# Kernel optimization log

Hardware: AMD Instinct MI355X
Metric: run time of the kernel (lower is better)

## Reference

```python
import jax, jax.numpy as jnp
import numpy as np

EPS = 1e-6

def setup_inputs() -> dict:
    key = jax.random.key(0)
    ks = jax.random.split(key, 6)
    N, E, Din, H, D = 50000, 800000, 256, 4, 32
    x = jax.random.normal(ks[0], (N, Din), dtype=jnp.float32)
    adj_indices = jax.random.randint(ks[1], (E, 2), 0, N, dtype=jnp.int32)
    adj_weights = jax.random.uniform(ks[2], (E,), dtype=jnp.float32)
    W = jax.random.normal(ks[3], (Din, H * D), dtype=jnp.float32) * (1.0 / np.sqrt(Din))
    a_src = jax.random.normal(ks[4], (H, D), dtype=jnp.float32)
    a_dst = jax.random.normal(ks[5], (H, D), dtype=jnp.float32)
    return {"x": x, "adj_indices": adj_indices, "adj_weights": adj_weights,
            "W": W, "a_src": a_src, "a_dst": a_dst}

def reference(x, adj_indices, adj_weights, W, a_src, a_dst):
    N = x.shape[0]
    H, D = a_src.shape
    h = (x @ W).reshape(N, H, D)                       # [N,H,D]
    src = adj_indices[:, 0]
    dst = adj_indices[:, 1]
    hs = h[src]                                        # [E,H,D]
    hd = h[dst]                                        # [E,H,D]
    raw = jnp.einsum('ehd,hd->eh', hs, a_src) + jnp.einsum('ehd,hd->eh', hd, a_dst)
    gate = jnp.clip(adj_weights, EPS, None)[:, None]   # [E,1]
    scores = jnp.tanh(raw) + jnp.log(gate)             # [E,H]
    # per-destination segment softmax (numerically stable)
    seg_max = jax.ops.segment_max(scores, dst, num_segments=N)   # [N,H]
    ex = jnp.exp(scores - seg_max[dst])
    denom = jax.ops.segment_sum(ex, dst, num_segments=N)         # [N,H]
    alpha = ex / denom[dst]                            # softmax over edges per dst
    alpha = alpha * gate
    messages = alpha[:, :, None] * hs                  # [E,H,D]
    out = jax.ops.segment_sum(messages, dst, num_segments=N)     # [N,H,D]
    out = out.reshape(N, H * D)
    return jax.nn.gelu(out, approximate=False)
```

## Files before the change

kernel.cpp:

```cpp
#include <hip/hip_runtime.h>
#include <hip/hip_bf16.h>

#define N_NODES 50000
#define N_EDGES 800000
#define DIN 256
#define HD 128
#define NH 4
#define CAP 64

#define GROWS 64
#define LDK 264

#define GEMM_BLOCKS ((N_NODES + GROWS - 1) / GROWS)
#define SCAT_BLOCKS ((N_EDGES + 255) / 256)

typedef __bf16 bf16x8 __attribute__((ext_vector_type(8)));
typedef float  f32x4  __attribute__((ext_vector_type(4)));

static __device__ __forceinline__ unsigned short f2bu(float v) {
  union { __hip_bfloat16 b; unsigned short u; } c;
  c.b = __float2bfloat16(v);
  return c.u;
}

__global__ void init_kernel(const float* __restrict__ W,
                            unsigned short* __restrict__ Wt,
                            int* __restrict__ cursor) {
  int i = blockIdx.x * 256 + threadIdx.x;
  if (i < HD * DIN) {
    int c = i >> 8, k = i & 255;
    Wt[c * 256 + k] = f2bu(W[k * HD + c]);
  }
  if (i < N_NODES) cursor[i] = 0;
}

__global__ __launch_bounds__(256, 2) void fused_gemm_scatter(
    const float* __restrict__ x,
    const unsigned short* __restrict__ Wt,
    const float* __restrict__ a_src,
    const float* __restrict__ a_dst,
    unsigned short* __restrict__ hbf,
    float* __restrict__ ssrc,
    float* __restrict__ sdst,
    const int2* __restrict__ adj,
    const float* __restrict__ wts,
    int* __restrict__ cursor,
    int2* __restrict__ slots) {
  __shared__ unsigned short xs[GROWS * LDK];
  const int tid = threadIdx.x;

  if (blockIdx.x >= GEMM_BLOCKS) {
    int e = (blockIdx.x - GEMM_BLOCKS) * 256 + tid;
    if (e >= N_EDGES) return;
    int2 sd = adj[e];
    if ((unsigned)sd.x >= (unsigned)N_NODES || (unsigned)sd.y >= (unsigned)N_NODES) return;
    float g = fmaxf(wts[e], 1e-6f);
    int pos = atomicAdd(&cursor[sd.y], 1);
    if (pos >= CAP) pos = CAP - 1;
    slots[((size_t)sd.y << 6) + pos] = make_int2(sd.x, __float_as_int(g));
    return;
  }

  const int row0 = blockIdx.x * GROWS;

#pragma unroll
  for (int it = 0; it < 16; it++) {
    int i  = it * 256 + tid;
    int r  = i >> 6;
    int kq = i & 63;
    int row = row0 + r;
    float4 v = make_float4(0.f, 0.f, 0.f, 0.f);
    if (row < N_NODES) v = *(const float4*)(x + (size_t)row * DIN + 4 * kq);
    ushort4 b;
    b.x = f2bu(v.x); b.y = f2bu(v.y); b.z = f2bu(v.z); b.w = f2bu(v.w);
    *(ushort4*)&xs[r * LDK + 4 * kq] = b;
  }
  __syncthreads();

  const int wid  = tid >> 6;
  const int lane = tid & 63;
  const int m    = lane & 15;
  const int q    = lane >> 4;

  f32x4 acc[8];
#pragma unroll
  for (int t = 0; t < 8; t++) acc[t] = (f32x4){0.f, 0.f, 0.f, 0.f};

  const unsigned short* xbase = &xs[(wid * 16 + m) * LDK];
#pragma unroll
  for (int s = 0; s < 8; s++) {
    bf16x8 afrag = *(const bf16x8*)(xbase + 32 * s + 8 * q);
#pragma unroll
    for (int t = 0; t < 8; t++) {
      bf16x8 bfrag = *(const bf16x8*)(Wt + (size_t)(16 * t + m) * 256 + 32 * s + 8 * q);
      acc[t] = __builtin_amdgcn_mfma_f32_16x16x32_bf16(afrag, bfrag, acc[t], 0, 0, 0);
    }
  }

#pragma unroll
  for (int t = 0; t < 8; t++) {
#pragma unroll
    for (int r = 0; r < 4; r++) {
      int row = row0 + wid * 16 + q * 4 + r;
      if (row < N_NODES) hbf[(size_t)row * HD + 16 * t + m] = f2bu(acc[t][r]);
    }
  }

  float as[8], ad[8];
#pragma unroll
  for (int t = 0; t < 8; t++) {
    as[t] = a_src[16 * t + m];
    ad[t] = a_dst[16 * t + m];
  }
#pragma unroll
  for (int r = 0; r < 4; r++) {
    float ps[NH] = {0.f, 0.f, 0.f, 0.f};
    float pd[NH] = {0.f, 0.f, 0.f, 0.f};
#pragma unroll
    for (int t = 0; t < 8; t++) {
      ps[t >> 1] = fmaf(acc[t][r], as[t], ps[t >> 1]);
      pd[t >> 1] = fmaf(acc[t][r], ad[t], pd[t >> 1]);
    }
#pragma unroll
    for (int mm = 8; mm >= 1; mm >>= 1) {
#pragma unroll
      for (int hh = 0; hh < NH; hh++) {
        ps[hh] += __shfl_xor(ps[hh], mm, 64);
        pd[hh] += __shfl_xor(pd[hh], mm, 64);
      }
    }
    int row = row0 + wid * 16 + q * 4 + r;
    if (m == 0 && row < N_NODES) {
#pragma unroll
      for (int hh = 0; hh < NH; hh++) {
        ssrc[row * NH + hh] = ps[hh];
        sdst[row * NH + hh] = pd[hh];
      }
    }
  }
}

__global__ void node_kernel(const int* __restrict__ cursor,
                            const int2* __restrict__ slots,
                            const float4* __restrict__ ssrc4,
                            const float4* __restrict__ sdst4,
                            const unsigned int* __restrict__ hbf32,
                            float* __restrict__ out) {
  const int tid  = threadIdx.x;
  const int wid  = tid >> 6;
  const int lane = tid & 63;
  const int n    = blockIdx.x * 2 + wid;
  const int hh   = lane >> 4;

  int deg = cursor[n];
  if (deg > CAP) deg = CAP;

  __shared__ float  sden[2][NH];
  __shared__ int    sidx[2][CAP];
  __shared__ float4 swv[2][CAP];
  if (lane < NH) sden[wid][lane] = 0.f;
  __syncthreads();

  if (lane < deg) {
    int2 sl = slots[((size_t)n << 6) + lane];
    int s = sl.x;
    float g = __int_as_float(sl.y);
    float4 ss = ssrc4[s];
    float4 sd = sdst4[n];
    float4 ex;
    ex.x = g * expf(tanhf(ss.x + sd.x));
    ex.y = g * expf(tanhf(ss.y + sd.y));
    ex.z = g * expf(tanhf(ss.z + sd.z));
    ex.w = g * expf(tanhf(ss.w + sd.w));
    sidx[wid][lane] = s;
    swv[wid][lane] = make_float4(ex.x * g, ex.y * g, ex.z * g, ex.w * g);
    atomicAdd(&sden[wid][0], ex.x);
    atomicAdd(&sden[wid][1], ex.y);
    atomicAdd(&sden[wid][2], ex.z);
    atomicAdd(&sden[wid][3], ex.w);
  }
  __syncthreads();

  float dn  = sden[wid][hh];
  float inv = (dn > 0.f) ? 1.f / dn : 0.f;

  float acc0 = 0.f, acc1 = 0.f;
  for (int j = 0; j < deg; j++) {
    float wj = ((const float*)&swv[wid][j])[hh];
    unsigned int u = hbf32[(size_t)sidx[wid][j] * (HD / 2) + lane];
    acc0 = fmaf(wj, __uint_as_float(u << 16), acc0);
    acc1 = fmaf(wj, __uint_as_float(u & 0xffff0000u), acc1);
  }
  acc0 *= inv;
  acc1 *= inv;

  float2 gl;
  gl.x = 0.5f * acc0 * (1.f + erff(acc0 * 0.70710678118654752f));
  gl.y = 0.5f * acc1 * (1.f + erff(acc1 * 0.70710678118654752f));
  *(float2*)&out[(size_t)n * HD + 2 * lane] = gl;
}

extern "C" void kernel_launch(void* const* d_in, const int* in_sizes, int n_in,
                              void* d_out, int out_size, void* d_ws, size_t ws_size,
                              hipStream_t stream) {
  const float* x     = (const float*)d_in[0];
  const int2*  adj   = (const int2*)d_in[1];
  const float* wts   = (const float*)d_in[2];
  const float* W     = (const float*)d_in[3];
  const float* a_src = (const float*)d_in[4];
  const float* a_dst = (const float*)d_in[5];
  float* out = (float*)d_out;

  char* p = (char*)d_ws;
  auto carve = [&](size_t bytes) {
    char* q = p;
    p += (bytes + 255) & ~(size_t)255;
    return (void*)q;
  };
  unsigned short* hbf = (unsigned short*)carve((size_t)N_NODES * HD * sizeof(unsigned short));
  unsigned short* Wt  = (unsigned short*)carve((size_t)HD * DIN * sizeof(unsigned short));
  float* ssrc   = (float*)carve((size_t)N_NODES * NH * sizeof(float));
  float* sdst   = (float*)carve((size_t)N_NODES * NH * sizeof(float));
  int2*  slots  = (int2*)carve((size_t)N_NODES * CAP * sizeof(int2));
  int*   cursor = (int*)carve((size_t)N_NODES * sizeof(int));

  init_kernel<<<(N_NODES + 255) / 256, 256, 0, stream>>>(W, Wt, cursor);
  fused_gemm_scatter<<<GEMM_BLOCKS + SCAT_BLOCKS, 256, 0, stream>>>(
      x, Wt, a_src, a_dst, hbf, ssrc, sdst, adj, wts, cursor, slots);
  node_kernel<<<N_NODES / 2, 128, 0, stream>>>(cursor, slots, (const float4*)ssrc,
                                               (const float4*)sdst,
                                               (const unsigned int*)hbf, out);
}
```

Measured before the change: 196.4 us.

## Halve GEMM LDS tile, pad cursor counters, shuffle-reduce denominators, unroll gather

Several independent changes. The GEMM stages x in two 128-wide K halves so LDS use drops and launch bounds rise to 8 blocks per CU for more occupancy, at the cost of an extra barrier per half. Per-node atomic cursors are spread to a 64-byte stride to cut atomic contention between neighbouring nodes, which makes the init kernel zero a 16x larger array. Node_kernel replaces LDS atomics and barriers with a wave shuffle reduction for the softmax denominator and unrolls the neighbor gather by 8 to keep more loads in flight.

```diff
diff --git a/kernel.cpp b/kernel.cpp
--- a/kernel.cpp
+++ b/kernel.cpp
@@ -7,9 +7,10 @@
 #define HD 128
 #define NH 4
 #define CAP 64
+#define CSTR 16
 
 #define GROWS 64
-#define LDK 264
+#define LDKH 136
 
 #define GEMM_BLOCKS ((N_NODES + GROWS - 1) / GROWS)
 #define SCAT_BLOCKS ((N_EDGES + 255) / 256)
@@ -31,10 +32,10 @@
     int c = i >> 8, k = i & 255;
     Wt[c * 256 + k] = f2bu(W[k * HD + c]);
   }
-  if (i < N_NODES) cursor[i] = 0;
-}
-
-__global__ __launch_bounds__(256, 2) void fused_gemm_scatter(
+  if (i < N_NODES * CSTR) cursor[i] = 0;
+}
+
+__global__ __launch_bounds__(256, 8) void fused_gemm_scatter(
     const float* __restrict__ x,
     const unsigned short* __restrict__ Wt,
     const float* __restrict__ a_src,
@@ -46,7 +47,7 @@
     const float* __restrict__ wts,
     int* __restrict__ cursor,
     int2* __restrict__ slots) {
-  __shared__ unsigned short xs[GROWS * LDK];
+  __shared__ unsigned short xs[GROWS * LDKH];
   const int tid = threadIdx.x;
 
   if (blockIdx.x >= GEMM_BLOCKS) {
@@ -55,28 +56,13 @@
     int2 sd = adj[e];
     if ((unsigned)sd.x >= (unsigned)N_NODES || (unsigned)sd.y >= (unsigned)N_NODES) return;
     float g = fmaxf(wts[e], 1e-6f);
-    int pos = atomicAdd(&cursor[sd.y], 1);
+    int pos = atomicAdd(&cursor[sd.y * CSTR], 1);
     if (pos >= CAP) pos = CAP - 1;
     slots[((size_t)sd.y << 6) + pos] = make_int2(sd.x, __float_as_int(g));
     return;
   }
 
   const int row0 = blockIdx.x * GROWS;
-
-#pragma unroll
-  for (int it = 0; it < 16; it++) {
-    int i  = it * 256 + tid;
-    int r  = i >> 6;
-    int kq = i & 63;
-    int row = row0 + r;
-    float4 v = make_float4(0.f, 0.f, 0.f, 0.f);
-    if (row < N_NODES) v = *(const float4*)(x + (size_t)row * DIN + 4 * kq);
-    ushort4 b;
-    b.x = f2bu(v.x); b.y = f2bu(v.y); b.z = f2bu(v.z); b.w = f2bu(v.w);
-    *(ushort4*)&xs[r * LDK + 4 * kq] = b;
-  }
-  __syncthreads();
-
   const int wid  = tid >> 6;
   const int lane = tid & 63;
   const int m    = lane & 15;
@@ -86,15 +72,33 @@
 #pragma unroll
   for (int t = 0; t < 8; t++) acc[t] = (f32x4){0.f, 0.f, 0.f, 0.f};
 
-  const unsigned short* xbase = &xs[(wid * 16 + m) * LDK];
-#pragma unroll
-  for (int s = 0; s < 8; s++) {
-    bf16x8 afrag = *(const bf16x8*)(xbase + 32 * s + 8 * q);
-#pragma unroll
-    for (int t = 0; t < 8; t++) {
-      bf16x8 bfrag = *(const bf16x8*)(Wt + (size_t)(16 * t + m) * 256 + 32 * s + 8 * q);
-      acc[t] = __builtin_amdgcn_mfma_f32_16x16x32_bf16(afrag, bfrag, acc[t], 0, 0, 0);
-    }
+#pragma unroll
+  for (int ks = 0; ks < 2; ks++) {
+#pragma unroll
+    for (int it = 0; it < 8; it++) {
+      int i  = it * 256 + tid;
+      int r  = i >> 5;
+      int kq = i & 31;
+      int row = row0 + r;
+      float4 v = make_float4(0.f, 0.f, 0.f, 0.f);
+      if (row < N_NODES) v = *(const float4*)(x + (size_t)row * DIN + ks * 128 + 4 * kq);
+      ushort4 b;
+      b.x = f2bu(v.x); b.y = f2bu(v.y); b.z = f2bu(v.z); b.w = f2bu(v.w);
+      *(ushort4*)&xs[r * LDKH + 4 * kq] = b;
+    }
+    __syncthreads();
+
+    const unsigned short* xbase = &xs[(wid * 16 + m) * LDKH];
+#pragma unroll
+    for (int s = 0; s < 4; s++) {
+      bf16x8 afrag = *(const bf16x8*)(xbase + 32 * s + 8 * q);
+#pragma unroll
+      for (int t = 0; t < 8; t++) {
+        bf16x8 bfrag = *(const bf16x8*)(Wt + (size_t)(16 * t + m) * 256 + ks * 128 + 32 * s + 8 * q);
+        acc[t] = __builtin_amdgcn_mfma_f32_16x16x32_bf16(afrag, bfrag, acc[t], 0, 0, 0);
+      }
+    }
+    __syncthreads();
   }
 
 #pragma unroll
@@ -140,56 +144,97 @@
   }
 }
 
-__global__ void node_kernel(const int* __restrict__ cursor,
-                            const int2* __restrict__ slots,
-                            const float4* __restrict__ ssrc4,
-                            const float4* __restrict__ sdst4,
-                            const unsigned int* __restrict__ hbf32,
-                            float* __restrict__ out) {
+__global__ __launch_bounds__(128, 8) void node_kernel(
+    const int* __restrict__ cursor,
+    const int2* __restrict__ slots,
+    const float4* __restrict__ ssrc4,
+    const float4* __restrict__ sdst4,
+    const unsigned int* __restrict__ hbf32,
+    float* __restrict__ out) {
   const int tid  = threadIdx.x;
   const int wid  = tid >> 6;
   const int lane = tid & 63;
   const int n    = blockIdx.x * 2 + wid;
   const int hh   = lane >> 4;
 
-  int deg = cursor[n];
+  int deg = cursor[n * CSTR];
   if (deg > CAP) deg = CAP;
 
-  __shared__ float  sden[2][NH];
   __shared__ int    sidx[2][CAP];
   __shared__ float4 swv[2][CAP];
-  if (lane < NH) sden[wid][lane] = 0.f;
-  __syncthreads();
-
+
+  float4 ex = make_float4(0.f, 0.f, 0.f, 0.f);
   if (lane < deg) {
     int2 sl = slots[((size_t)n << 6) + lane];
     int s = sl.x;
     float g = __int_as_float(sl.y);
     float4 ss = ssrc4[s];
     float4 sd = sdst4[n];
-    float4 ex;
     ex.x = g * expf(tanhf(ss.x + sd.x));
     ex.y = g * expf(tanhf(ss.y + sd.y));
     ex.z = g * expf(tanhf(ss.z + sd.z));
     ex.w = g * expf(tanhf(ss.w + sd.w));
     sidx[wid][lane] = s;
     swv[wid][lane] = make_float4(ex.x * g, ex.y * g, ex.z * g, ex.w * g);
-    atomicAdd(&sden[wid][0], ex.x);
-    atomicAdd(&sden[wid][1], ex.y);
-    atomicAdd(&sden[wid][2], ex.z);
-    atomicAdd(&sden[wid][3], ex.w);
-  }
-  __syncthreads();
-
-  float dn  = sden[wid][hh];
+  }
+
+  float4 tot = ex;
+#pragma unroll
+  for (int mm = 32; mm >= 1; mm >>= 1) {
+    tot.x += __shfl_xor(tot.x, mm, 64);
+    tot.y += __shfl_xor(tot.y, mm, 64);
+    tot.z += __shfl_xor(tot.z, mm, 64);
+    tot.w += __shfl_xor(tot.w, mm, 64);
+  }
+  float dn  = (hh == 0) ? tot.x : (hh == 1) ? tot.y : (hh == 2) ? tot.z : tot.w;
   float inv = (dn > 0.f) ? 1.f / dn : 0.f;
 
   float acc0 = 0.f, acc1 = 0.f;
-  for (int j = 0; j < deg; j++) {
-    float wj = ((const float*)&swv[wid][j])[hh];
-    unsigned int u = hbf32[(size_t)sidx[wid][j] * (HD / 2) + lane];
-    acc0 = fmaf(wj, __uint_as_float(u << 16), acc0);
-    acc1 = fmaf(wj, __uint_as_float(u & 0xffff0000u), acc1);
+  int j = 0;
+  for (; j + 8 <= deg; j += 8) {
+    int s0 = sidx[wid][j + 0], s1 = sidx[wid][j + 1];
+    int s2 = sidx[wid][j + 2], s3 = sidx[wid][j + 3];
+    int s4 = sidx[wid][j + 4], s5 = sidx[wid][j + 5];
+    int s6 = sidx[wid][j + 6], s7 = sidx[wid][j + 7];
+    unsigned u0 = hbf32[(size_t)s0 * (HD / 2) + lane];
+    unsigned u1 = hbf32[(size_t)s1 * (HD / 2) + lane];
+    unsigned u2 = hbf32[(size_t)s2 * (HD / 2) + lane];
+    unsigned u3 = hbf32[(size_t)s3 * (HD / 2) + lane];
+    unsigned u4 = hbf32[(size_t)s4 * (HD / 2) + lane];
+    unsigned u5 = hbf32[(size_t)s5 * (HD / 2) + lane];
+    unsigned u6 = hbf32[(size_t)s6 * (HD / 2) + lane];
+    unsigned u7 = hbf32[(size_t)s7 * (HD / 2) + lane];
+    float w0 = ((const float*)&swv[wid][j + 0])[hh];
+    float w1 = ((const float*)&swv[wid][j + 1])[hh];
+    float w2 = ((const float*)&swv[wid][j + 2])[hh];
+    float w3 = ((const float*)&swv[wid][j + 3])[hh];
+    float w4 = ((const float*)&swv[wid][j + 4])[hh];
+    float w5 = ((const float*)&swv[wid][j + 5])[hh];
+    float w6 = ((const float*)&swv[wid][j + 6])[hh];
+    float w7 = ((const float*)&swv[wid][j + 7])[hh];
+    acc0 = fmaf(w0, __uint_as_float(u0 << 16), acc0);
+    acc1 = fmaf(w0, __uint_as_float(u0 & 0xffff0000u), acc1);
+    acc0 = fmaf(w1, __uint_as_float(u1 << 16), acc0);
+    acc1 = fmaf(w1, __uint_as_float(u1 & 0xffff0000u), acc1);
+    acc0 = fmaf(w2, __uint_as_float(u2 << 16), acc0);
+    acc1 = fmaf(w2, __uint_as_float(u2 & 0xffff0000u), acc1);
+    acc0 = fmaf(w3, __uint_as_float(u3 << 16), acc0);
+    acc1 = fmaf(w3, __uint_as_float(u3 & 0xffff0000u), acc1);
+    acc0 = fmaf(w4, __uint_as_float(u4 << 16), acc0);
+    acc1 = fmaf(w4, __uint_as_float(u4 & 0xffff0000u), acc1);
+    acc0 = fmaf(w5, __uint_as_float(u5 << 16), acc0);
+    acc1 = fmaf(w5, __uint_as_float(u5 & 0xffff0000u), acc1);
+    acc0 = fmaf(w6, __uint_as_float(u6 << 16), acc0);
+    acc1 = fmaf(w6, __uint_as_float(u6 & 0xffff0000u), acc1);
+    acc0 = fmaf(w7, __uint_as_float(u7 << 16), acc0);
+    acc1 = fmaf(w7, __uint_as_float(u7 & 0xffff0000u), acc1);
+  }
+  for (; j < deg; j++) {
+    int s0 = sidx[wid][j];
+    unsigned u0 = hbf32[(size_t)s0 * (HD / 2) + lane];
+    float w0 = ((const float*)&swv[wid][j])[hh];
+    acc0 = fmaf(w0, __uint_as_float(u0 << 16), acc0);
+    acc1 = fmaf(w0, __uint_as_float(u0 & 0xffff0000u), acc1);
   }
   acc0 *= inv;
   acc1 *= inv;
@@ -222,9 +267,9 @@
   float* ssrc   = (float*)carve((size_t)N_NODES * NH * sizeof(float));
   float* sdst   = (float*)carve((size_t)N_NODES * NH * sizeof(float));
   int2*  slots  = (int2*)carve((size_t)N_NODES * CAP * sizeof(int2));
-  int*   cursor = (int*)carve((size_t)N_NODES * sizeof(int));
-
-  init_kernel<<<(N_NODES + 255) / 256, 256, 0, stream>>>(W, Wt, cursor);
+  int*   cursor = (int*)carve((size_t)N_NODES * CSTR * sizeof(int));
+
+  init_kernel<<<(N_NODES * CSTR + 255) / 256, 256, 0, stream>>>(W, Wt, cursor);
   fused_gemm_scatter<<<GEMM_BLOCKS + SCAT_BLOCKS, 256, 0, stream>>>(
       x, Wt, a_src, a_dst, hbf, ssrc, sdst, adj, wts, cursor, slots);
   node_kernel<<<N_NODES / 2, 128, 0, stream>>>(cursor, slots, (const float4*)ssrc,
```

Measured after the change: 263.6 us. 34.2% more time.
